# Performance work log

Measured on AMD Instinct MI355X. Metric: run time of the kernel, lower is better.

The kernel has to match this reference:

```python
import jax, jax.numpy as jnp
import numpy as np

# 16-joint kinematic tree (index 0 = root); child i depends on PARENTS[i]
PARENTS = [0, 0, 1, 2, 3, 1, 5, 6, 1, 8, 9, 10, 8, 12, 13, 14]
NUM_LAYERS = 2
H = 1024          # output_size = input_size + bridge_size
B = 256           # batch
D = 512           # input_size == bridge_size


def setup_inputs() -> dict:
    key = jax.random.key(0)
    ks = jax.random.split(key, 6)
    n_nodes = len(PARENTS) - 1  # 15 non-root joints
    s = 1.0 / np.sqrt(H).astype(np.float32)  # torch LSTM init scale
    return {
        "input": jax.random.normal(ks[0], (n_nodes, B, D), jnp.float32),
        "bridge": jax.random.normal(ks[1], (n_nodes, B, D), jnp.float32),
        "W_ih": jax.random.normal(ks[2], (NUM_LAYERS, 4 * H, H), jnp.float32) * s,
        "W_hh": jax.random.normal(ks[3], (NUM_LAYERS, 4 * H, H), jnp.float32) * s,
        "b_ih": jax.random.normal(ks[4], (NUM_LAYERS, 4 * H), jnp.float32) * s,
        "b_hh": jax.random.normal(ks[5], (NUM_LAYERS, 4 * H), jnp.float32) * s,
    }


def _lstm_cell(x, h, c, Wih, Whh, bih, bhh):
    # gates: [B, 4H], torch gate order i, f, g, o
    g = x @ Wih.T + h @ Whh.T + (bih + bhh)
    i, f, gg, o = jnp.split(g, 4, axis=-1)
    c_new = jax.nn.sigmoid(f) * c + jax.nn.sigmoid(i) * jnp.tanh(gg)
    h_new = jax.nn.sigmoid(o) * jnp.tanh(c_new)
    return h_new, c_new


def reference(input, bridge, W_ih, W_hh, b_ih, b_hh):
    # batch_first=False: inputs are [n_nodes, B, D]; concat -> feature H = 2D
    x_all = jnp.concatenate([input, bridge], axis=-1)   # [n_nodes, B, H]
    x_all = jnp.transpose(x_all, (1, 0, 2))             # [B, n_nodes, H]
    batch = x_all.shape[0]
    zero = jnp.zeros((NUM_LAYERS, batch, H), x_all.dtype)
    hs, cs = [zero], [zero]  # root joint starts with zero state
    outs = []
    # serial walk over the fixed, small kinematic tree (15 joints)
    for j in range(1, len(PARENTS)):
        ph, pc = hs[PARENTS[j]], cs[PARENTS[j]]
        x = x_all[:, j - 1]
        new_h, new_c = [], []
        for l in range(NUM_LAYERS):
            h, c = _lstm_cell(x, ph[l], pc[l], W_ih[l], W_hh[l], b_ih[l], b_hh[l])
            new_h.append(h)
            new_c.append(c)
            x = h  # top layer output feeds next layer / becomes joint output
        outs.append(x)
        hs.append(jnp.stack(new_h))
        cs.append(jnp.stack(new_c))
    out = jnp.stack(outs, axis=1)          # [B, n_nodes, H]
    return jnp.transpose(out, (1, 0, 2))   # back to seq-first [n_nodes, B, H]
```

## Files before the change

### kernel.cpp

```cpp
#include <hip/hip_runtime.h>
#include <stdint.h>

typedef unsigned short u16;
typedef uint32_t u32;
typedef short s16x8 __attribute__((ext_vector_type(8)));
typedef float fx16 __attribute__((ext_vector_type(16)));

#define B_   256
#define H_   1024
#define BH_  (B_ * H_)
#define WPE  ((size_t)2 * 4096 * 2048)
#define XPE  ((size_t)15 * BH_)
#define HPE  ((size_t)32 * BH_)
#define NT   32
#define SLOT 24576

struct Stage { int node[8]; int par[8]; int layer[8]; int cnt; };

__device__ __forceinline__ u16 bf16_rn(float x) {
    union { float f; u32 u; } v; v.f = x;
    return (u16)((v.u + 0x7FFFu + ((v.u >> 16) & 1u)) >> 16);
}
__device__ __forceinline__ float sigf(float x) {
    return __builtin_amdgcn_rcpf(1.0f + __expf(-x));
}
__device__ __forceinline__ float tanh_f(float x) {
    return 1.0f - 2.0f * __builtin_amdgcn_rcpf(1.0f + __expf(2.0f * x));
}

__global__ __launch_bounds__(256)
void pack_weights(const float* __restrict__ Wih, const float* __restrict__ Whh,
                  u16* __restrict__ wp)
{
    const int gt = blockIdx.x * 256 + threadIdx.x;
    const int w = gt >> 6, lane = gt & 63;
    const int k16 = w & 127, cg = (w >> 7) & 31, gate = (w >> 12) & 3, layer = w >> 14;
    const int row = gate * 1024 + cg * 32 + (lane & 31);
    const int k = k16 * 16 + (lane >> 5) * 8;
    const float* src = (k < 1024)
        ? Wih + ((size_t)layer * 4096 + row) * 1024 + k
        : Whh + ((size_t)layer * 4096 + row) * 1024 + (k - 1024);
    const float4 v0 = *(const float4*)src;
    const float4 v1 = *(const float4*)(src + 4);
    const float a[8] = {v0.x, v0.y, v0.z, v0.w, v1.x, v1.y, v1.z, v1.w};
    union { u16 s[8]; uint4 v; } hi;
    #pragma unroll
    for (int e = 0; e < 8; ++e) hi.s[e] = bf16_rn(a[e]);
    *(uint4*)(wp + (size_t)w * 512 + (size_t)lane * 8) = hi.v;
}

__global__ __launch_bounds__(256)
void pack_x(const float* __restrict__ input, const float* __restrict__ bridge,
            u16* __restrict__ xp)
{
    const int gt = blockIdx.x * 256 + threadIdx.x;
    const int w = gt >> 6, lane = gt & 63;
    const int k16 = w & 63, btile = (w >> 6) & 7, n1 = w >> 9;
    const int b = btile * 32 + (lane & 31);
    const int k = k16 * 16 + (lane >> 5) * 8;
    const float* src = (k < 512)
        ? input  + ((size_t)n1 * 256 + b) * 512 + k
        : bridge + ((size_t)n1 * 256 + b) * 512 + (k - 512);
    const float4 v0 = *(const float4*)src;
    const float4 v1 = *(const float4*)(src + 4);
    const float a[8] = {v0.x, v0.y, v0.z, v0.w, v1.x, v1.y, v1.z, v1.w};
    union { u16 s[8]; uint4 v; } hi;
    #pragma unroll
    for (int e = 0; e < 8; ++e) hi.s[e] = bf16_rn(a[e]);
    *(uint4*)(xp + (size_t)w * 512 + (size_t)lane * 8) = hi.v;
}

__global__ __launch_bounds__(256)
void bias_sum_k(const float* __restrict__ bih, const float* __restrict__ bhh,
                float* __restrict__ bs)
{
    const int i = blockIdx.x * 256 + threadIdx.x;
    if (i < 8192) bs[i] = bih[i] + bhh[i];
}

__global__ __launch_bounds__(512, 1)
void cell_fused(const u16* __restrict__ wp, const u16* __restrict__ xp,
                u16* __restrict__ hp, float* __restrict__ c_buf,
                const float* __restrict__ bsum, float* __restrict__ out,
                Stage st)
{
    __shared__ u16 SM[3 * SLOT];

    const int bid  = blockIdx.x;
    const int cell = bid >> 5;
    const int u    = bid & 31;
    const int hhblk = 4 * (u & 7) + (u >> 3);
    const int node = st.node[cell], par = st.par[cell], layer = st.layer[cell];
    const int tid = threadIdx.x, wv = tid >> 6, lane = tid & 63;
    const int tq  = tid >> 8;
    const int kks = (tid >> 6) & 3;
    const int e8  = (tid & 63) * 8;

    const u16 *A0, *A1;
    if (layer == 0) {
        A0 = xp + (size_t)(node - 1) * BH_;
        A1 = hp + (size_t)(par * 2 + 0) * BH_;
    } else {
        A0 = hp + (size_t)(node * 2 + 0) * BH_;
        A1 = hp + (size_t)(par * 2 + 1) * BH_;
    }
    size_t wsg[2];
    #pragma unroll
    for (int i = 0; i < 2; ++i)
        wsg[i] = (size_t)((layer * 4 + (2 * i + tq)) * 32 + hhblk) * 65536
               + (size_t)kks * 512 + e8;

    #define STAGE(T, S) do {                                                   \
        const u16* As_ = ((T) < 16) ? A0 : A1;                                 \
        const size_t ab_ = ((size_t)((T) & 15) * 4 + kks) * 512 + e8;          \
        _Pragma("unroll")                                                      \
        for (int i_ = 0; i_ < 4; ++i_) {                                       \
            __builtin_amdgcn_global_load_lds(                                  \
                (const __attribute__((address_space(1))) void*)                \
                    (As_ + (size_t)(2 * i_ + tq) * 32768 + ab_),               \
                (__attribute__((address_space(3))) void*)                      \
                    (SM + (S) * SLOT + i_ * 4096 + tid * 8),                   \
                16, 0, 0);                                                     \
        }                                                                      \
        _Pragma("unroll")                                                      \
        for (int i_ = 0; i_ < 2; ++i_) {                                       \
            __builtin_amdgcn_global_load_lds(                                  \
                (const __attribute__((address_space(1))) void*)                \
                    (wp + wsg[i_] + (size_t)(T) * 2048),                       \
                (__attribute__((address_space(3))) void*)                      \
                    (SM + (S) * SLOT + 16384 + i_ * 4096 + tid * 8),           \
                16, 0, 0);                                                     \
        }                                                                      \
    } while (0)

    #define COMPUTE(S) do {                                                    \
        _Pragma("unroll")                                                      \
        for (int kk_ = 0; kk_ < 4; ++kk_) {                                    \
            const s16x8 a_ = *(const s16x8*)                                   \
                (SM + (S) * SLOT + wv * 2048 + kk_ * 512 + lane * 8);          \
            _Pragma("unroll")                                                  \
            for (int g_ = 0; g_ < 4; ++g_) {                                   \
                const s16x8 w_ = *(const s16x8*)                               \
                    (SM + (S) * SLOT + 16384 + g_ * 2048 + kk_ * 512           \
                     + lane * 8);                                              \
                acc[g_] = __builtin_amdgcn_mfma_f32_32x32x16_bf16(             \
                    a_, w_, acc[g_], 0, 0, 0);                                 \
            }                                                                  \
        }                                                                      \
    } while (0)

    fx16 acc[4];
    #pragma unroll
    for (int g = 0; g < 4; ++g)
        #pragma unroll
        for (int r = 0; r < 16; ++r) acc[g][r] = 0.0f;

    STAGE(0, 0);
    STAGE(1, 1);

    #pragma unroll 1
    for (int t = 0; t < NT; ++t) {
        asm volatile("s_waitcnt vmcnt(6)" ::: "memory");
        __builtin_amdgcn_s_barrier();
        const int sT = (t + 2 < NT) ? (t + 2) : (NT - 1);
        STAGE(sT, (t + 2) % 3);
        COMPUTE(t % 3);
    }
    __syncthreads();

    const int col  = lane & 31;
    const int colg = hhblk * 32 + col;
    float bs4[4];
    #pragma unroll
    for (int g = 0; g < 4; ++g)
        bs4[g] = bsum[layer * 4096 + g * 1024 + colg];

    const float* cpar = c_buf + (size_t)(par * 2 + layer) * BH_ + colg;
    float*       cnew = c_buf + (size_t)(node * 2 + layer) * BH_ + colg;
    float*       outp = out + (size_t)(node - 1) * BH_ + colg;
    u16*         hpn  = hp + (size_t)(node * 2 + layer) * BH_;

    u32* hq = (u32*)(&SM[0]) + wv * 1056;

    #pragma unroll
    for (int r = 0; r < 16; ++r) {
        const int rl = 4 * (lane >> 5) + (r & 3) + 8 * (r >> 2);
        const size_t row = (size_t)(wv * 32 + rl) * 1024;
        const float gi = acc[0][r] + bs4[0];
        const float gf = acc[1][r] + bs4[1];
        const float gg = acc[2][r] + bs4[2];
        const float go = acc[3][r] + bs4[3];
        const float cp = cpar[row];
        const float cn = sigf(gf) * cp + sigf(gi) * tanh_f(gg);
        const float hn = sigf(go) * tanh_f(cn);
        cnew[row] = cn;
        if (layer == 1) outp[row] = hn;
        hq[rl * 33 + col] = (u32)bf16_rn(hn);
    }

    #pragma unroll
    for (int q = 0; q < 2; ++q) {
        const int k16h = hhblk * 2 + q;
        union { u16 s[8]; uint4 v; } pk;
        #pragma unroll
        for (int e = 0; e < 8; ++e)
            pk.s[e] = (u16)hq[(lane & 31) * 33 + q * 16 + (lane >> 5) * 8 + e];
        *(uint4*)(hpn + ((size_t)wv * 64 + k16h) * 512 + lane * 8) = pk.v;
    }
    #undef STAGE
    #undef COMPUTE
}

extern "C" void kernel_launch(void* const* d_in, const int* in_sizes, int n_in,
                              void* d_out, int out_size, void* d_ws, size_t ws_size,
                              hipStream_t stream)
{
    const float* input  = (const float*)d_in[0];
    const float* bridge = (const float*)d_in[1];
    const float* Wih    = (const float*)d_in[2];
    const float* Whh    = (const float*)d_in[3];
    const float* bih    = (const float*)d_in[4];
    const float* bhh    = (const float*)d_in[5];
    float* out = (float*)d_out;

    u16* wp = (u16*)d_ws;
    u16* xp = wp + WPE;
    u16* hp = xp + XPE;
    float* c_buf = (float*)(hp + HPE);
    float* bsum  = c_buf + HPE;

    hipMemsetAsync(hp, 0, (size_t)2 * BH_ * sizeof(u16), stream);
    hipMemsetAsync(c_buf, 0, (size_t)2 * BH_ * sizeof(float), stream);

    bias_sum_k<<<32, 256, 0, stream>>>(bih, bhh, bsum);
    pack_weights<<<8192, 256, 0, stream>>>(Wih, Whh, wp);
    pack_x<<<1920, 256, 0, stream>>>(input, bridge, xp);

    static const Stage stages[7] = {
        { {1},                      {0},                      {0},                      1 },
        { {1,2,5,8},                {0,1,1,1},                {1,0,0,0},                4 },
        { {2,5,8,3,6,9,12},         {1,1,1,2,5,8,8},          {1,1,1,0,0,0,0},          7 },
        { {3,6,9,12,4,7,10,13},     {2,5,8,8,3,6,9,12},       {1,1,1,1,0,0,0,0},        8 },
        { {4,7,10,13,11,14},        {3,6,9,12,10,13},         {1,1,1,1,0,0},            6 },
        { {11,14,15},               {10,13,14},               {1,1,0},                  3 },
        { {15},                     {14},                     {1},                      1 },
    };

    for (int s = 0; s < 7; ++s) {
        cell_fused<<<dim3(stages[s].cnt * 32), 512, 0, stream>>>(
            wp, xp, hp, c_buf, bsum, out, stages[s]);
    }
}
```

Baseline: 299.1 us.

## Split LSTM gate GEMM into x/h halves with partial-sum planes and flags

Each cell's gate GEMM is split into an input half and a recurrent half. All 15 layer-0 input projections are precomputed in the first launch, and the layer-1 input halves are computed concurrently with dependent work, written as fp32 partial planes and signalled via per-block release flags. The consumer blocks spin on the acquire flags, add the partial sums, then run the cell epilogue. This shortens the serial critical path and spreads more blocks per launch. In exchange it adds partial-plane memory traffic, drops the 3-stage LDS pipeline for a single-buffered loop, and risks deadlock if producer and consumer blocks are not co-resident.

```diff
diff --git a/kernel.cpp b/kernel.cpp
--- a/kernel.cpp
+++ b/kernel.cpp
@@ -12,10 +12,13 @@
 #define WPE  ((size_t)2 * 4096 * 2048)
 #define XPE  ((size_t)15 * BH_)
 #define HPE  ((size_t)32 * BH_)
-#define NT   32
-#define SLOT 24576
-
-struct Stage { int node[8]; int par[8]; int layer[8]; int cnt; };
+#define NTH  16
+#define GPLANE ((size_t)B_ * 4096)
+
+struct StageEx {
+    signed char node[16], par[16], layer[16], mode[16], slot[16];
+    int cnt;
+};
 
 __device__ __forceinline__ u16 bf16_rn(float x) {
     union { float f; u32 u; } v; v.f = x;
@@ -78,76 +81,38 @@
     if (i < 8192) bs[i] = bih[i] + bhh[i];
 }
 
-__global__ __launch_bounds__(512, 1)
-void cell_fused(const u16* __restrict__ wp, const u16* __restrict__ xp,
-                u16* __restrict__ hp, float* __restrict__ c_buf,
-                const float* __restrict__ bsum, float* __restrict__ out,
-                Stage st)
-{
-    __shared__ u16 SM[3 * SLOT];
+__global__ __launch_bounds__(512, 4)
+void cell_half(const u16* __restrict__ wp, const u16* __restrict__ xp,
+               u16* __restrict__ hp, float* __restrict__ c_buf,
+               const float* __restrict__ bsum, float* __restrict__ out,
+               float* __restrict__ gpart, int* __restrict__ flags,
+               StageEx st)
+{
+    __shared__ u16 SM[24576];
 
     const int bid  = blockIdx.x;
-    const int cell = bid >> 5;
+    const int item = bid >> 5;
     const int u    = bid & 31;
     const int hhblk = 4 * (u & 7) + (u >> 3);
-    const int node = st.node[cell], par = st.par[cell], layer = st.layer[cell];
+    const int node  = st.node[item], par = st.par[item];
+    const int layer = st.layer[item], mode = st.mode[item], slot = st.slot[item];
+    const int seg   = (mode == 2) ? 1 : 0;
+
     const int tid = threadIdx.x, wv = tid >> 6, lane = tid & 63;
     const int tq  = tid >> 8;
     const int kks = (tid >> 6) & 3;
     const int e8  = (tid & 63) * 8;
 
-    const u16 *A0, *A1;
-    if (layer == 0) {
-        A0 = xp + (size_t)(node - 1) * BH_;
-        A1 = hp + (size_t)(par * 2 + 0) * BH_;
-    } else {
-        A0 = hp + (size_t)(node * 2 + 0) * BH_;
-        A1 = hp + (size_t)(par * 2 + 1) * BH_;
-    }
+    const u16* Ab;
+    if (mode == 2) Ab = hp + (size_t)(par * 2 + layer) * BH_;
+    else           Ab = layer ? hp + (size_t)(node * 2) * BH_
+                              : xp + (size_t)(node - 1) * BH_;
+
     size_t wsg[2];
     #pragma unroll
     for (int i = 0; i < 2; ++i)
         wsg[i] = (size_t)((layer * 4 + (2 * i + tq)) * 32 + hhblk) * 65536
-               + (size_t)kks * 512 + e8;
-
-    #define STAGE(T, S) do {                                                   \
-        const u16* As_ = ((T) < 16) ? A0 : A1;                                 \
-        const size_t ab_ = ((size_t)((T) & 15) * 4 + kks) * 512 + e8;          \
-        _Pragma("unroll")                                                      \
-        for (int i_ = 0; i_ < 4; ++i_) {                                       \
-            __builtin_amdgcn_global_load_lds(                                  \
-                (const __attribute__((address_space(1))) void*)                \
-                    (As_ + (size_t)(2 * i_ + tq) * 32768 + ab_),               \
-                (__attribute__((address_space(3))) void*)                      \
-                    (SM + (S) * SLOT + i_ * 4096 + tid * 8),                   \
-                16, 0, 0);                                                     \
-        }                                                                      \
-        _Pragma("unroll")                                                      \
-        for (int i_ = 0; i_ < 2; ++i_) {                                       \
-            __builtin_amdgcn_global_load_lds(                                  \
-                (const __attribute__((address_space(1))) void*)                \
-                    (wp + wsg[i_] + (size_t)(T) * 2048),                       \
-                (__attribute__((address_space(3))) void*)                      \
-                    (SM + (S) * SLOT + 16384 + i_ * 4096 + tid * 8),           \
-                16, 0, 0);                                                     \
-        }                                                                      \
-    } while (0)
-
-    #define COMPUTE(S) do {                                                    \
-        _Pragma("unroll")                                                      \
-        for (int kk_ = 0; kk_ < 4; ++kk_) {                                    \
-            const s16x8 a_ = *(const s16x8*)                                   \
-                (SM + (S) * SLOT + wv * 2048 + kk_ * 512 + lane * 8);          \
-            _Pragma("unroll")                                                  \
-            for (int g_ = 0; g_ < 4; ++g_) {                                   \
-                const s16x8 w_ = *(const s16x8*)                               \
-                    (SM + (S) * SLOT + 16384 + g_ * 2048 + kk_ * 512           \
-                     + lane * 8);                                              \
-                acc[g_] = __builtin_amdgcn_mfma_f32_32x32x16_bf16(             \
-                    a_, w_, acc[g_], 0, 0, 0);                                 \
-            }                                                                  \
-        }                                                                      \
-    } while (0)
+               + (size_t)seg * 32768 + (size_t)kks * 512 + e8;
 
     fx16 acc[4];
     #pragma unroll
@@ -155,21 +120,76 @@
         #pragma unroll
         for (int r = 0; r < 16; ++r) acc[g][r] = 0.0f;
 
-    STAGE(0, 0);
-    STAGE(1, 1);
-
     #pragma unroll 1
-    for (int t = 0; t < NT; ++t) {
-        asm volatile("s_waitcnt vmcnt(6)" ::: "memory");
-        __builtin_amdgcn_s_barrier();
-        const int sT = (t + 2 < NT) ? (t + 2) : (NT - 1);
-        STAGE(sT, (t + 2) % 3);
-        COMPUTE(t % 3);
-    }
-    __syncthreads();
+    for (int t = 0; t < NTH; ++t) {
+        const size_t ab = ((size_t)t * 4 + kks) * 512 + e8;
+        #pragma unroll
+        for (int i = 0; i < 4; ++i) {
+            __builtin_amdgcn_global_load_lds(
+                (const __attribute__((address_space(1))) void*)
+                    (Ab + (size_t)(2 * i + tq) * 32768 + ab),
+                (__attribute__((address_space(3))) void*)
+                    (SM + i * 4096 + tid * 8),
+                16, 0, 0);
+        }
+        #pragma unroll
+        for (int i = 0; i < 2; ++i) {
+            __builtin_amdgcn_global_load_lds(
+                (const __attribute__((address_space(1))) void*)
+                    (wp + wsg[i] + (size_t)t * 2048),
+                (__attribute__((address_space(3))) void*)
+                    (SM + 16384 + i * 4096 + tid * 8),
+                16, 0, 0);
+        }
+        __syncthreads();
+        #pragma unroll
+        for (int kk = 0; kk < 4; ++kk) {
+            const s16x8 a_ = *(const s16x8*)(SM + wv * 2048 + kk * 512 + lane * 8);
+            #pragma unroll
+            for (int g = 0; g < 4; ++g) {
+                const s16x8 w_ = *(const s16x8*)
+                    (SM + 16384 + g * 2048 + kk * 512 + lane * 8);
+                acc[g] = __builtin_amdgcn_mfma_f32_32x32x16_bf16(
+                    a_, w_, acc[g], 0, 0, 0);
+            }
+        }
+        __syncthreads();
+    }
 
     const int col  = lane & 31;
     const int colg = hhblk * 32 + col;
+
+    if (mode == 0) {
+        float* gp = gpart + (size_t)slot * GPLANE;
+        #pragma unroll
+        for (int r = 0; r < 16; ++r) {
+            const int rl  = 4 * (lane >> 5) + (r & 3) + 8 * (r >> 2);
+            const size_t row = (size_t)(wv * 32 + rl) * 4096;
+            #pragma unroll
+            for (int g = 0; g < 4; ++g)
+                gp[row + g * 1024 + colg] = acc[g][r];
+        }
+        if (layer == 1) {
+            __syncthreads();
+            if (tid == 0)
+                __hip_atomic_store(flags + (node * 32 + u) * 32, 1,
+                                   __ATOMIC_RELEASE, __HIP_MEMORY_SCOPE_AGENT);
+        }
+        return;
+    }
+
+    const float* pp = (mode == 2) ? gpart + (size_t)slot * GPLANE : nullptr;
+    if (mode == 2 && layer == 1) {
+        if (tid == 0) {
+            while (__hip_atomic_load(flags + (node * 32 + u) * 32,
+                                     __ATOMIC_ACQUIRE,
+                                     __HIP_MEMORY_SCOPE_AGENT) < 1) {
+                __builtin_amdgcn_s_sleep(4);
+            }
+        }
+        __syncthreads();
+    }
+
     float bs4[4];
     #pragma unroll
     for (int g = 0; g < 4; ++g)
@@ -186,13 +206,16 @@
     for (int r = 0; r < 16; ++r) {
         const int rl = 4 * (lane >> 5) + (r & 3) + 8 * (r >> 2);
         const size_t row = (size_t)(wv * 32 + rl) * 1024;
-        const float gi = acc[0][r] + bs4[0];
-        const float gf = acc[1][r] + bs4[1];
-        const float gg = acc[2][r] + bs4[2];
-        const float go = acc[3][r] + bs4[3];
+        float gv[4];
+        #pragma unroll
+        for (int g = 0; g < 4; ++g) {
+            gv[g] = acc[g][r] + bs4[g];
+            if (mode == 2)
+                gv[g] += pp[(size_t)(wv * 32 + rl) * 4096 + g * 1024 + colg];
+        }
         const float cp = cpar[row];
-        const float cn = sigf(gf) * cp + sigf(gi) * tanh_f(gg);
-        const float hn = sigf(go) * tanh_f(cn);
+        const float cn = sigf(gv[1]) * cp + sigf(gv[0]) * tanh_f(gv[2]);
+        const float hn = sigf(gv[3]) * tanh_f(cn);
         cnew[row] = cn;
         if (layer == 1) outp[row] = hn;
         hq[rl * 33 + col] = (u32)bf16_rn(hn);
@@ -207,8 +230,6 @@
             pk.s[e] = (u16)hq[(lane & 31) * 33 + q * 16 + (lane >> 5) * 8 + e];
         *(uint4*)(hpn + ((size_t)wv * 64 + k16h) * 512 + lane * 8) = pk.v;
     }
-    #undef STAGE
-    #undef COMPUTE
 }
 
 extern "C" void kernel_launch(void* const* d_in, const int* in_sizes, int n_in,
@@ -228,26 +249,49 @@
     u16* hp = xp + XPE;
     float* c_buf = (float*)(hp + HPE);
     float* bsum  = c_buf + HPE;
+    float* gpart = bsum + 8192;
+    int*   flags = (int*)(gpart + (size_t)19 * GPLANE);
 
     hipMemsetAsync(hp, 0, (size_t)2 * BH_ * sizeof(u16), stream);
     hipMemsetAsync(c_buf, 0, (size_t)2 * BH_ * sizeof(float), stream);
+    hipMemsetAsync(flags, 0, 16384 * sizeof(int), stream);
 
     bias_sum_k<<<32, 256, 0, stream>>>(bih, bhh, bsum);
     pack_weights<<<8192, 256, 0, stream>>>(Wih, Whh, wp);
     pack_x<<<1920, 256, 0, stream>>>(input, bridge, xp);
 
-    static const Stage stages[7] = {
-        { {1},                      {0},                      {0},                      1 },
-        { {1,2,5,8},                {0,1,1,1},                {1,0,0,0},                4 },
-        { {2,5,8,3,6,9,12},         {1,1,1,2,5,8,8},          {1,1,1,0,0,0,0},          7 },
-        { {3,6,9,12,4,7,10,13},     {2,5,8,8,3,6,9,12},       {1,1,1,1,0,0,0,0},        8 },
-        { {4,7,10,13,11,14},        {3,6,9,12,10,13},         {1,1,1,1,0,0},            6 },
-        { {11,14,15},               {10,13,14},               {1,1,0},                  3 },
-        { {15},                     {14},                     {1},                      1 },
+    static const StageEx S[7] = {
+        { {1,2,3,4,5,6,7,8,9,10,11,12,13,14,15},
+          {0,1,2,3,1,5,6,1,8,9,10,8,12,13,14},
+          {0,0,0,0,0,0,0,0,0,0,0,0,0,0,0},
+          {1,0,0,0,0,0,0,0,0,0,0,0,0,0,0},
+          {0,1,2,3,4,5,6,7,8,9,10,11,12,13,14}, 15 },
+        { {1,2,5,8}, {0,1,1,1}, {1,0,0,0}, {1,2,2,2}, {0,1,4,7}, 4 },
+        { {2,5,8, 2,5,8, 3,6,9,12},
+          {1,1,1, 1,1,1, 2,5,8,8},
+          {1,1,1, 1,1,1, 0,0,0,0},
+          {0,0,0, 2,2,2, 2,2,2,2},
+          {15,16,17, 15,16,17, 2,5,8,11}, 10 },
+        { {3,6,9,12, 3,6,9,12, 4,7,10,13},
+          {2,5,8,8,  2,5,8,8,  3,6,9,12},
+          {1,1,1,1,  1,1,1,1,  0,0,0,0},
+          {0,0,0,0,  2,2,2,2,  2,2,2,2},
+          {15,16,17,18, 15,16,17,18, 3,6,9,12}, 12 },
+        { {4,7,10,13, 4,7,10,13, 11,14},
+          {3,6,9,12,  3,6,9,12,  10,13},
+          {1,1,1,1,   1,1,1,1,   0,0},
+          {0,0,0,0,   2,2,2,2,   2,2},
+          {15,16,17,18, 15,16,17,18, 10,13}, 10 },
+        { {11,14, 11,14, 15},
+          {10,13, 10,13, 14},
+          {1,1,   1,1,   0},
+          {0,0,   2,2,   2},
+          {15,16, 15,16, 14}, 5 },
+        { {15,15}, {14,14}, {1,1}, {0,2}, {15,15}, 2 },
     };
 
     for (int s = 0; s < 7; ++s) {
-        cell_fused<<<dim3(stages[s].cnt * 32), 512, 0, stream>>>(
-            wp, xp, hp, c_buf, bsum, out, stages[s]);
-    }
-}
+        cell_half<<<dim3(S[s].cnt * 32), 512, 0, stream>>>(
+            wp, xp, hp, c_buf, bsum, out, gpart, flags, S[s]);
+    }
+}
```

Result: slower. 460.9 us (+54.1%).
